# Optimization experiments

Hardware: AMD Instinct MI355X
Metric: run time of the kernel (lower is better)

The kernel has to match this reference:

```python
import jax, jax.numpy as jnp
import numpy as np

B, C, H, W = 8, 4, 768, 768
MIN_SIZE = 50          # unused on the keep_largest=True path, matching the torch module
KEEP_LARGEST = True
INF = H * W + 2        # sentinel label for background pixels


def setup_inputs() -> dict:
    key = jax.random.key(0)
    pred = jax.random.normal(key, (B, C, H, W), dtype=jnp.float32)
    return {"pred": pred}


def _ccl_keep_largest(mask):
    """4-connected components of a (H, W) bool mask; returns float mask of the
    largest component (ties broken by smallest raster-order seed label, matching
    np.argmax over scipy.ndimage.label sizes). Empty mask -> all zeros."""
    idx = jnp.arange(1, H * W + 1, dtype=jnp.int32).reshape(H, W)

    def prop(l):
        # min over 4-neighborhood, restricted to foreground pixels
        p = jnp.pad(l, 1, constant_values=INF)
        n = jnp.minimum(jnp.minimum(p[:-2, 1:-1], p[2:, 1:-1]),
                        jnp.minimum(p[1:-1, :-2], p[1:-1, 2:]))
        return jnp.where(mask, jnp.minimum(l, n), INF)

    l0 = jnp.where(mask, idx, INF)
    l1 = prop(l0)

    def cond(c):
        cur, prev = c
        return jnp.any(cur != prev)

    def body(c):
        cur, _ = c
        return prop(cur), cur

    l, _ = jax.lax.while_loop(cond, body, (l1, l0))
    # fixed point: each foreground pixel holds the min seed index of its component
    labels = jnp.where(mask, l, 0)  # 0 = background

    sizes = jax.ops.segment_sum(jnp.ones(H * W, jnp.int32), labels.ravel(),
                                num_segments=H * W + 1)
    sizes = sizes.at[0].set(0)  # exclude background
    if KEEP_LARGEST:
        largest = jnp.argmax(sizes)
        keep = (labels == largest) & (sizes[largest] > 0)
    else:
        good = sizes >= MIN_SIZE
        keep = good[labels] & (labels > 0)
    return keep.astype(jnp.float32)


def reference(pred):
    pred_labels = jnp.argmax(pred, axis=1)  # (B, H, W)
    classes = jnp.arange(1, C)
    # (B, C-1, H, W) binary masks for classes 1..C-1
    masks = pred_labels[:, None, :, :] == classes[None, :, None, None]
    fg = jax.vmap(_ccl_keep_largest)(masks.reshape(-1, H, W)).reshape(B, C - 1, H, W)
    bg = 1.0 - jnp.clip(fg.sum(axis=1), 0.0, 1.0)
    return jnp.concatenate([bg[:, None], fg], axis=1)  # (B, C, H, W)
```

## Files before the change

### kernel.cpp

```cpp
#include <hip/hip_runtime.h>
#include <stdint.h>


constexpr int BB    = 8;
constexpr int CC    = 4;
constexpr int HH    = 768;
constexpr int WW    = 768;
constexpr int HWP   = HH * WW;
constexpr int NMASK = BB * (CC - 1);
constexpr int TPB   = 256;
constexpr int NBLK  = HWP / TPB;
constexpr int NBLK4 = HWP / (4 * TPB);

constexpr int SLAB_ROWS = 4;
constexpr int SLAB_PIX  = SLAB_ROWS * WW;
constexpr int NSLAB     = HH / SLAB_ROWS;
constexpr int GR_SLAB   = SLAB_PIX / 4;
constexpr int NBOUND    = (NSLAB - 1) * WW;
constexpr int NBLK_BR   = (NBOUND + TPB - 1) / TPB;

constexpr int CSH  = 20;
constexpr int LMSK = (1 << CSH) - 1;
constexpr int LSH  = 12;
constexpr int LLMSK = (1 << LSH) - 1;

__device__ __forceinline__ int findroot(const int* __restrict__ P, int x) {
  int l = P[x] & LMSK;
  while (l != x) { x = l; l = P[x] & LMSK; }
  return x;
}

__device__ __forceinline__ void unite(int* P, int a, int b, int cls) {
  a = findroot(P, a);
  b = findroot(P, b);
  while (a != b) {
    if (a < b) { int t = a; a = b; b = t; }
    int old = atomicMin(&P[a], (cls << CSH) | b);
    if ((old & LMSK) == a) return;
    a = findroot(P, old & LMSK);
    b = findroot(P, b);
  }
}

__global__ void __launch_bounds__(TPB)
k_init(const float* __restrict__ pred, int* __restrict__ parent,
       float* __restrict__ out) {
  __shared__ int lp[SLAB_PIX];
  int s = blockIdx.x;
  int b = blockIdx.y;
  int t = threadIdx.x;
  const float4* base = (const float4*)(pred + (size_t)b * CC * HWP);
  int4* cntz = (int4*)(out + (size_t)(b * CC + 1) * HWP);
  int4 z4 = make_int4(0, 0, 0, 0);

  unsigned char am[3][4];
#pragma unroll
  for (int i = 0; i < 3; ++i) {
    int g = s * GR_SLAB + i * TPB + t;
    float4 v0 = base[g];
    float4 v1 = base[(size_t)(HWP / 4) + g];
    float4 v2 = base[(size_t)(HWP / 4) * 2 + g];
    float4 v3 = base[(size_t)(HWP / 4) * 3 + g];
    float c0[4] = {v0.x, v0.y, v0.z, v0.w};
    float c1[4] = {v1.x, v1.y, v1.z, v1.w};
    float c2[4] = {v2.x, v2.y, v2.z, v2.w};
    float c3[4] = {v3.x, v3.y, v3.z, v3.w};
#pragma unroll
    for (int j = 0; j < 4; ++j) {
      float bv = c0[j]; int a = 0;
      if (c1[j] > bv) { bv = c1[j]; a = 1; }
      if (c2[j] > bv) { bv = c2[j]; a = 2; }
      if (c3[j] > bv) { bv = c3[j]; a = 3; }
      am[i][j] = (unsigned char)a;
    }
    cntz[g] = z4;
    int l0 = (i * TPB + t) * 4;
    int4 iv;
    iv.x = am[i][0] ? ((int)am[i][0] << LSH) | l0       : -1;
    iv.y = am[i][1] ? ((int)am[i][1] << LSH) | (l0 + 1) : -1;
    iv.z = am[i][2] ? ((int)am[i][2] << LSH) | (l0 + 2) : -1;
    iv.w = am[i][3] ? ((int)am[i][3] << LSH) | (l0 + 3) : -1;
    *(int4*)&lp[l0] = iv;
  }

  auto lfind = [&](int x) {
    int l = lp[x] & LLMSK;
    while (l != x) { x = l; l = lp[x] & LLMSK; }
    return x;
  };
  auto lunite = [&](int a, int c, int cls) {
    a = lfind(a); c = lfind(c);
    while (a != c) {
      if (a < c) { int tmp = a; a = c; c = tmp; }
      int old = atomicMin(&lp[a], (cls << LSH) | c);
      if ((old & LLMSK) == a) return;
      a = lfind(old & LLMSK);
      c = lfind(c);
    }
  };

  __syncthreads();
#pragma unroll
  for (int i = 0; i < 3; ++i) {
    int l0   = (i * TPB + t) * 4;
    int row  = l0 / WW;
    int col0 = l0 - row * WW;
#pragma unroll
    for (int j = 0; j < 4; ++j) {
      int l = l0 + j;
      int cls = am[i][j];
      if (!cls) continue;
      if (col0 + j + 1 < WW) {
        int nv = lp[l + 1];
        if (nv >= 0 && (nv >> LSH) == cls) lunite(l, l + 1, cls);
      }
      if (row < SLAB_ROWS - 1) {
        int nv = lp[l + WW];
        if (nv >= 0 && (nv >> LSH) == cls) lunite(l, l + WW, cls);
      }
    }
  }
  __syncthreads();
  int gbase = s * SLAB_PIX;
  int* Pb = parent + (size_t)b * HWP;
#pragma unroll
  for (int i = 0; i < 3; ++i) {
    int l0 = (i * TPB + t) * 4;
    int4 pv;
    pv.x = (lp[l0]     >= 0) ? ((lp[l0]     >> LSH) << CSH) | (gbase + lfind(l0))     : -1;
    pv.y = (lp[l0 + 1] >= 0) ? ((lp[l0 + 1] >> LSH) << CSH) | (gbase + lfind(l0 + 1)) : -1;
    pv.z = (lp[l0 + 2] >= 0) ? ((lp[l0 + 2] >> LSH) << CSH) | (gbase + lfind(l0 + 2)) : -1;
    pv.w = (lp[l0 + 3] >= 0) ? ((lp[l0 + 3] >> LSH) << CSH) | (gbase + lfind(l0 + 3)) : -1;
    ((int4*)Pb)[s * GR_SLAB + i * TPB + t] = pv;
  }
}

__global__ void __launch_bounds__(TPB)
k_bridge(int* __restrict__ parent) {
  int bp = blockIdx.x * TPB + threadIdx.x;
  if (bp >= NBOUND) return;
  int* P = parent + (size_t)blockIdx.y * HWP;
  int k = bp / WW;
  int x = bp - k * WW;
  int p = (SLAB_ROWS * k + SLAB_ROWS - 1) * WW + x;
  int pv = P[p], qv = P[p + WW];
  if (pv >= 0 && qv >= 0 && ((pv ^ qv) >> CSH) == 0)
    unite(P, p, p + WW, pv >> CSH);
}

__global__ void __launch_bounds__(TPB)
k_flatten_count(int* __restrict__ parent, float* __restrict__ out,
                unsigned long long* __restrict__ blockmax) {
  int pix = blockIdx.x * TPB + threadIdx.x;
  int b   = blockIdx.y;
  int* P  = parent + (size_t)b * HWP;
  int pv  = P[pix];
  int r = -1, cls = 0;
  if (pv >= 0) {
    cls = pv >> CSH;
    int lbl = pv & LMSK;
    r = (lbl == pix) ? pix : findroot(P, lbl);
    if (r != lbl) P[pix] = (cls << CSH) | r;
  }
  int lane = threadIdx.x & 63;
  int prev = __shfl_up(r, 1);
  bool bound = (lane == 0) || (prev != r);
  unsigned long long lb = __ballot(bound);
  unsigned long long pack = 0ull;
  if (bound && r >= 0) {
    unsigned long long rest = (lane == 63) ? 0ull : (lb >> (lane + 1));
    int nxt = rest ? (lane + 1 + (int)__builtin_ctzll(rest)) : 64;
    int len = nxt - lane;
    uint32_t* cnt = (uint32_t*)(out + (size_t)(b * CC + 1) * HWP);
    uint32_t old = atomicAdd(cnt + r, (uint32_t)len);
    pack = (((unsigned long long)(old + (uint32_t)len)) << 32) |
           (unsigned long long)(0xFFFFFFFFu - (uint32_t)r);
  }
  __shared__ unsigned long long sm[3][TPB / 64];
  int wid = threadIdx.x >> 6;
#pragma unroll
  for (int cm = 0; cm < 3; ++cm) {
    unsigned long long pc = (cls == cm + 1) ? pack : 0ull;
#pragma unroll
    for (int off = 32; off > 0; off >>= 1) {
      unsigned long long o = __shfl_down(pc, off);
      if (o > pc) pc = o;
    }
    if (lane == 0) sm[cm][wid] = pc;
  }
  __syncthreads();
  if (threadIdx.x < 3) {
    int cm = threadIdx.x;
    unsigned long long bm = sm[cm][0];
#pragma unroll
    for (int i = 1; i < TPB / 64; ++i) if (sm[cm][i] > bm) bm = sm[cm][i];
    blockmax[(size_t)(b * 3 + cm) * NBLK + blockIdx.x] = bm;
  }
}

__global__ void __launch_bounds__(TPB)
k_reduce_best(const unsigned long long* __restrict__ blockmax,
              unsigned long long* __restrict__ best) {
  int m = blockIdx.x;
  const unsigned long long* bm = blockmax + (size_t)m * NBLK;
  unsigned long long v = 0ull;
  for (int i = threadIdx.x; i < NBLK; i += TPB) {
    unsigned long long o = bm[i];
    if (o > v) v = o;
  }
#pragma unroll
  for (int off = 32; off > 0; off >>= 1) {
    unsigned long long o = __shfl_down(v, off);
    if (o > v) v = o;
  }
  __shared__ unsigned long long sm[TPB / 64];
  int lane = threadIdx.x & 63, wid = threadIdx.x >> 6;
  if (lane == 0) sm[wid] = v;
  __syncthreads();
  if (threadIdx.x == 0) {
    unsigned long long b0 = sm[0];
#pragma unroll
    for (int i = 1; i < TPB / 64; ++i) if (sm[i] > b0) b0 = sm[i];
    best[m] = b0;
  }
}

__global__ void __launch_bounds__(TPB)
k_final(const int* __restrict__ parent, const unsigned long long* __restrict__ best,
        float* __restrict__ out) {
  int g = blockIdx.x * TPB + threadIdx.x;
  int b = blockIdx.y;
  int broot[3];
#pragma unroll
  for (int cm = 0; cm < 3; ++cm) {
    unsigned long long bv = best[b * 3 + cm];
    broot[cm] = (bv >> 32) ? (int)(0xFFFFFFFFu - (uint32_t)bv) : -2;
  }
  int4 pv = ((const int4*)(parent + (size_t)b * HWP))[g];
  int pvs[4] = {pv.x, pv.y, pv.z, pv.w};
  float4 ch[4];
  float* chf = (float*)ch;
#pragma unroll
  for (int c = 0; c < 4; ++c) ch[c] = make_float4(0.f, 0.f, 0.f, 0.f);
#pragma unroll
  for (int j = 0; j < 4; ++j) {
    int v = pvs[j];
    if (v >= 0) {
      int cls = v >> CSH;
      bool match = (v & LMSK) == broot[cls - 1];
      chf[cls * 4 + j] = match ? 1.f : 0.f;
      chf[j]           = match ? 0.f : 1.f;
    } else {
      chf[j] = 1.f;
    }
  }
  float4* ob = (float4*)(out + (size_t)b * CC * HWP);
#pragma unroll
  for (int c = 0; c < 4; ++c)
    ob[(size_t)(HWP / 4) * c + g] = ch[c];
}

extern "C" void kernel_launch(void* const* d_in, const int* in_sizes, int n_in,
                              void* d_out, int out_size, void* d_ws, size_t ws_size,
                              hipStream_t stream) {
  const float* pred = (const float*)d_in[0];
  float* out = (float*)d_out;

  int* parent = (int*)d_ws;
  unsigned long long* best =
      (unsigned long long*)((char*)d_ws + (size_t)BB * HWP * sizeof(int));
  unsigned long long* blockmax = (unsigned long long*)(out + (size_t)2 * HWP);

  dim3 blk(TPB);
  k_init          <<<dim3(NSLAB, BB),   blk, 0, stream>>>(pred, parent, out);
  k_bridge        <<<dim3(NBLK_BR, BB), blk, 0, stream>>>(parent);
  k_flatten_count <<<dim3(NBLK, BB),    blk, 0, stream>>>(parent, out, blockmax);
  k_reduce_best   <<<dim3(NMASK),       blk, 0, stream>>>(blockmax, best);
  k_final         <<<dim3(NBLK4, BB),   blk, 0, stream>>>(parent, best, out);
}
```

Before: 224.1 us.

## Pre-label horizontal runs via wave scan and prune redundant vertical unions

In the slab-local init kernel, each wave now computes the run start of equal-class horizontal runs using a shuffle-based max prefix scan, so pixels start already linked to their run head. This removes the per-pixel horizontal union-find calls. Vertical unions are skipped when the left neighbour and the lower-left neighbour already share the class, because that connection is implied. Wave-boundary runs are joined by lane 0. k_final also processes two int4 groups per thread with half as many blocks. The cost is the extra shuffle work and some added complexity in the init phase.

```diff
diff --git a/kernel.cpp b/kernel.cpp
--- a/kernel.cpp
+++ b/kernel.cpp
@@ -10,7 +10,7 @@
 constexpr int NMASK = BB * (CC - 1);
 constexpr int TPB   = 256;
 constexpr int NBLK  = HWP / TPB;
-constexpr int NBLK4 = HWP / (4 * TPB);
+constexpr int NBLK8 = HWP / (8 * TPB);
 
 constexpr int SLAB_ROWS = 4;
 constexpr int SLAB_PIX  = SLAB_ROWS * WW;
@@ -49,6 +49,7 @@
   int s = blockIdx.x;
   int b = blockIdx.y;
   int t = threadIdx.x;
+  int lane = t & 63;
   const float4* base = (const float4*)(pred + (size_t)b * CC * HWP);
   int4* cntz = (int4*)(out + (size_t)(b * CC + 1) * HWP);
   int4 z4 = make_int4(0, 0, 0, 0);
@@ -74,12 +75,33 @@
       am[i][j] = (unsigned char)a;
     }
     cntz[g] = z4;
-    int l0 = (i * TPB + t) * 4;
+
+    int cls0 = am[i][0], cls1 = am[i][1], cls2 = am[i][2], cls3 = am[i][3];
+    int c4pk = cls0 | (cls1 << 2) | (cls2 << 4) | (cls3 << 6);
+    int prevl = __shfl_up(c4pk, 1) >> 6;
+    bool b0 = (lane == 0) || (cls0 != (prevl & 3));
+    bool b1 = cls1 != cls0;
+    bool b2 = cls2 != cls1;
+    bool b3 = cls3 != cls2;
+    int lb = b3 ? 3 : (b2 ? 2 : (b1 ? 1 : (b0 ? 0 : -1)));
+    int v = (lb >= 0) ? lane * 4 + lb : -1;
+#pragma unroll
+    for (int off = 1; off < 64; off <<= 1) {
+      int o = __shfl_up(v, off);
+      if (lane >= off && o > v) v = o;
+    }
+    int ex = __shfl_up(v, 1);
+    int rs0 = b0 ? lane * 4     : ex;
+    int rs1 = b1 ? lane * 4 + 1 : rs0;
+    int rs2 = b2 ? lane * 4 + 2 : rs1;
+    int rs3 = b3 ? lane * 4 + 3 : rs2;
+    int seg = i * 1024 + (t >> 6) * 256;
+    int l0  = seg + lane * 4;
     int4 iv;
-    iv.x = am[i][0] ? ((int)am[i][0] << LSH) | l0       : -1;
-    iv.y = am[i][1] ? ((int)am[i][1] << LSH) | (l0 + 1) : -1;
-    iv.z = am[i][2] ? ((int)am[i][2] << LSH) | (l0 + 2) : -1;
-    iv.w = am[i][3] ? ((int)am[i][3] << LSH) | (l0 + 3) : -1;
+    iv.x = cls0 ? (cls0 << LSH) | (seg + rs0) : -1;
+    iv.y = cls1 ? (cls1 << LSH) | (seg + rs1) : -1;
+    iv.z = cls2 ? (cls2 << LSH) | (seg + rs2) : -1;
+    iv.w = cls3 ? (cls3 << LSH) | (seg + rs3) : -1;
     *(int4*)&lp[l0] = iv;
   }
 
@@ -100,24 +122,39 @@
   };
 
   __syncthreads();
+
+  if (lane == 0) {
+#pragma unroll
+    for (int i = 0; i < 3; ++i) {
+      int seg = i * 1024 + (t >> 6) * 256;
+      int cls = am[i][0];
+      if (cls && (seg % WW) != 0) {
+        int nv = lp[seg - 1];
+        if (nv >= 0 && (nv >> LSH) == cls) lunite(seg, seg - 1, cls);
+      }
+    }
+  }
 #pragma unroll
   for (int i = 0; i < 3; ++i) {
     int l0   = (i * TPB + t) * 4;
     int row  = l0 / WW;
     int col0 = l0 - row * WW;
+    if (row == SLAB_ROWS - 1) continue;
 #pragma unroll
     for (int j = 0; j < 4; ++j) {
-      int l = l0 + j;
       int cls = am[i][j];
       if (!cls) continue;
-      if (col0 + j + 1 < WW) {
-        int nv = lp[l + 1];
-        if (nv >= 0 && (nv >> LSH) == cls) lunite(l, l + 1, cls);
+      int l = l0 + j;
+      int nv = lp[l + WW];
+      if (nv < 0 || (nv >> LSH) != cls) continue;
+      if (col0 + j > 0) {
+        int lv = lp[l - 1];
+        if (lv >= 0 && (lv >> LSH) == cls) {
+          int bv = lp[l + WW - 1];
+          if (bv >= 0 && (bv >> LSH) == cls) continue;
+        }
       }
-      if (row < SLAB_ROWS - 1) {
-        int nv = lp[l + WW];
-        if (nv >= 0 && (nv >> LSH) == cls) lunite(l, l + WW, cls);
-      }
+      lunite(l, l + WW, cls);
     }
   }
   __syncthreads();
@@ -228,7 +265,6 @@
 __global__ void __launch_bounds__(TPB)
 k_final(const int* __restrict__ parent, const unsigned long long* __restrict__ best,
         float* __restrict__ out) {
-  int g = blockIdx.x * TPB + threadIdx.x;
   int b = blockIdx.y;
   int broot[3];
 #pragma unroll
@@ -236,28 +272,33 @@
     unsigned long long bv = best[b * 3 + cm];
     broot[cm] = (bv >> 32) ? (int)(0xFFFFFFFFu - (uint32_t)bv) : -2;
   }
-  int4 pv = ((const int4*)(parent + (size_t)b * HWP))[g];
-  int pvs[4] = {pv.x, pv.y, pv.z, pv.w};
-  float4 ch[4];
-  float* chf = (float*)ch;
-#pragma unroll
-  for (int c = 0; c < 4; ++c) ch[c] = make_float4(0.f, 0.f, 0.f, 0.f);
-#pragma unroll
-  for (int j = 0; j < 4; ++j) {
-    int v = pvs[j];
-    if (v >= 0) {
-      int cls = v >> CSH;
-      bool match = (v & LMSK) == broot[cls - 1];
-      chf[cls * 4 + j] = match ? 1.f : 0.f;
-      chf[j]           = match ? 0.f : 1.f;
-    } else {
-      chf[j] = 1.f;
-    }
-  }
+  const int4* Pb = (const int4*)(parent + (size_t)b * HWP);
   float4* ob = (float4*)(out + (size_t)b * CC * HWP);
 #pragma unroll
-  for (int c = 0; c < 4; ++c)
-    ob[(size_t)(HWP / 4) * c + g] = ch[c];
+  for (int h = 0; h < 2; ++h) {
+    int g = blockIdx.x * (2 * TPB) + h * TPB + threadIdx.x;
+    int4 pv = Pb[g];
+    int pvs[4] = {pv.x, pv.y, pv.z, pv.w};
+    float4 ch[4];
+    float* chf = (float*)ch;
+#pragma unroll
+    for (int c = 0; c < 4; ++c) ch[c] = make_float4(0.f, 0.f, 0.f, 0.f);
+#pragma unroll
+    for (int j = 0; j < 4; ++j) {
+      int v = pvs[j];
+      if (v >= 0) {
+        int cls = v >> CSH;
+        bool match = (v & LMSK) == broot[cls - 1];
+        chf[cls * 4 + j] = match ? 1.f : 0.f;
+        chf[j]           = match ? 0.f : 1.f;
+      } else {
+        chf[j] = 1.f;
+      }
+    }
+#pragma unroll
+    for (int c = 0; c < 4; ++c)
+      ob[(size_t)(HWP / 4) * c + g] = ch[c];
+  }
 }
 
 extern "C" void kernel_launch(void* const* d_in, const int* in_sizes, int n_in,
@@ -276,5 +317,5 @@
   k_bridge        <<<dim3(NBLK_BR, BB), blk, 0, stream>>>(parent);
   k_flatten_count <<<dim3(NBLK, BB),    blk, 0, stream>>>(parent, out, blockmax);
   k_reduce_best   <<<dim3(NMASK),       blk, 0, stream>>>(blockmax, best);
-  k_final         <<<dim3(NBLK4, BB),   blk, 0, stream>>>(parent, best, out);
-}
+  k_final         <<<dim3(NBLK8, BB),   blk, 0, stream>>>(parent, best, out);
+}
```

Measured after the change: 221.0 us. About the same (-1.4%).
